# Optimization experiments

Hardware: AMD Instinct MI355X
Metric: run time of the kernel (lower is better)

The kernel has to match this reference:

```python
import jax, jax.numpy as jnp
import numpy as np

S, B, D_MODEL, H, DH = 2048, 2, 1024, 16, 64
FACTOR = 1.0 / np.sqrt(DH).astype(np.float32)


def setup_inputs() -> dict:
    key = jax.random.key(0)
    ks = jax.random.split(key, 12)
    sc = 0.02
    inp = {
        'query': jax.random.normal(ks[0], (S, B, D_MODEL), jnp.float32),
        'key': jax.random.normal(ks[1], (S, B, D_MODEL), jnp.float32),
        'value': jax.random.normal(ks[2], (S, B, D_MODEL), jnp.float32),
        # causal mask [seq_q, seq_k, 1]; 0 -> masked
        'mask': jnp.tril(jnp.ones((S, S), dtype=bool))[:, :, None],
        'Wq': jax.random.normal(ks[3], (H * DH, D_MODEL), jnp.float32) * sc,
        'bq': jnp.zeros((H * DH,), jnp.float32),
        'Wk': jax.random.normal(ks[4], (H * DH, D_MODEL), jnp.float32) * sc,
        'bk': jnp.zeros((H * DH,), jnp.float32),
        'Wv': jax.random.normal(ks[5], (H * DH, D_MODEL), jnp.float32) * sc,
        'bv': jnp.zeros((H * DH,), jnp.float32),
        'Wo': jax.random.normal(ks[6], (D_MODEL, H * DH), jnp.float32) * sc,
        'bo': jnp.zeros((D_MODEL,), jnp.float32),
    }
    return inp


def _split_heads(x):
    # pattern: 's b (head_dim head_num) -> s b head_num head_dim' (head_dim is OUTER)
    s, b, _ = x.shape
    return x.reshape(s, b, DH, H).transpose(0, 1, 3, 2)  # [s,b,H,DH]


def reference(query, key, value, mask, Wq, bq, Wk, bk, Wv, bv, Wo, bo):
    q = _split_heads(query @ Wq.T + bq)
    k = _split_heads(key @ Wk.T + bk)
    v = _split_heads(value @ Wv.T + bv)
    scores = jnp.einsum('ibhd,jbhd->ijbh', q, k) * FACTOR  # [i,j,b,h]
    scores = jnp.where(mask[..., None], scores, -jnp.inf)
    attn = jax.nn.softmax(scores, axis=1)  # softmax over keys (dim=1)
    out = jnp.einsum('ijbh,jbhd->ibhd', attn, v)  # [i,b,h,d]
    out = out.reshape(S, B, H * DH)  # 'i b h d -> i b (h d)'
    return out @ Wo.T + bo
```

## Files before the change

kernel.cpp:

```cpp
#include <hip/hip_runtime.h>


typedef float f32x4 __attribute__((ext_vector_type(4)));
typedef float f32x16 __attribute__((ext_vector_type(16)));
typedef __bf16 bf16x8_t __attribute__((ext_vector_type(8)));
typedef unsigned short ushort8 __attribute__((ext_vector_type(8)));
typedef unsigned int uint4v __attribute__((ext_vector_type(4)));
typedef unsigned int uint2v __attribute__((ext_vector_type(2)));

#define S_LEN 2048
#define BATCH 2
#define DMODEL 1024
#define NHEAD 16
#define DHEAD 64
#define K_SCALE 0.18033688011112042f

__device__ __forceinline__ unsigned short f2bf(float x) {
  unsigned int u = __builtin_bit_cast(unsigned int, x);
  u += 0x7fffu + ((u >> 16) & 1u);
  return (unsigned short)(u >> 16);
}

__device__ __forceinline__ f32x4 mfma16(ushort8 a, ushort8 b, f32x4 c) {
  return __builtin_amdgcn_mfma_f32_16x16x32_bf16(
      __builtin_bit_cast(bf16x8_t, a), __builtin_bit_cast(bf16x8_t, b), c, 0, 0, 0);
}
__device__ __forceinline__ f32x16 mfma32(ushort8 a, ushort8 b, f32x16 c) {
  return __builtin_amdgcn_mfma_f32_32x32x16_bf16(
      __builtin_bit_cast(bf16x8_t, a), __builtin_bit_cast(bf16x8_t, b), c, 0, 0, 0);
}

__device__ __forceinline__ ushort8 pack8(float4 a, float4 b, float s) {
  ushort8 t;
  t[0] = f2bf(a.x * s); t[1] = f2bf(a.y * s); t[2] = f2bf(a.z * s); t[3] = f2bf(a.w * s);
  t[4] = f2bf(b.x * s); t[5] = f2bf(b.y * s); t[6] = f2bf(b.z * s); t[7] = f2bf(b.w * s);
  return t;
}

__device__ __forceinline__ void gload16(unsigned short* lds, const unsigned short* g) {
  __builtin_amdgcn_global_load_lds(
      (const __attribute__((address_space(1))) unsigned int*)g,
      (__attribute__((address_space(3))) unsigned int*)lds, 16, 0, 0);
}

__global__ __launch_bounds__(256) void cvt_kernel(
    const float* __restrict__ q, const float* __restrict__ k, const float* __restrict__ v,
    const float* __restrict__ wq, const float* __restrict__ wk,
    const float* __restrict__ wv, const float* __restrict__ wo,
    unsigned short* __restrict__ qB, unsigned short* __restrict__ kB,
    unsigned short* __restrict__ vB, unsigned short* __restrict__ wqB,
    unsigned short* __restrict__ wkB, unsigned short* __restrict__ wvB,
    unsigned short* __restrict__ woB)
{
  const int c = blockIdx.x * 256 + threadIdx.x;
  const float* s; unsigned short* d; int base;
  if      (c < 524288)  { s = q;  d = qB;  base = 0; }
  else if (c < 1048576) { s = k;  d = kB;  base = 524288; }
  else if (c < 1572864) { s = v;  d = vB;  base = 1048576; }
  else if (c < 1703936) { s = wq; d = wqB; base = 1572864; }
  else if (c < 1835008) { s = wk; d = wkB; base = 1703936; }
  else if (c < 1966080) { s = wv; d = wvB; base = 1835008; }
  else                  { s = wo; d = woB; base = 1966080; }
  const size_t off = (size_t)(c - base) * 8;
  const float4 v0 = *reinterpret_cast<const float4*>(s + off);
  const float4 v1 = *reinterpret_cast<const float4*>(s + off + 4);
  *reinterpret_cast<ushort8*>(d + off) = pack8(v0, v1, 1.0f);
}

template<bool OUTBF16>
__global__ __launch_bounds__(256) void gemm_bf16_kernel(
    const unsigned short* __restrict__ A, const unsigned short* __restrict__ W,
    const float* __restrict__ bias, void* __restrict__ Cv, float oscale)
{
  __shared__ __align__(16) unsigned short As[2][128 * 64];
  __shared__ __align__(16) unsigned short Ws[2][64 * 64];
  const int tid = threadIdx.x;
  const int lane = tid & 63;
  const int w = tid >> 6;
  const int wm = (w >> 1) * 64, wn = (w & 1) * 32;
  const int g = lane >> 4, lr = lane & 15;

  const int bid = (int)blockIdx.x;
  const int widx = (bid & 7) * 64 + (bid >> 3);
  const int n0 = (widx & 15) * 64;
  const int m0 = (widx >> 4) * 128;

  f32x4 acc[4][2] = {};

#define STAGE(buf, k0)                                                              \
  {                                                                                 \
    _Pragma("unroll")                                                               \
    for (int ii = 0; ii < 4; ++ii) {                                                \
      const int c = ii * 256 + tid;                                                 \
      const int row = c >> 3;                                                       \
      const int sl = (c & 7) ^ (row & 7);                                           \
      gload16(&As[buf][c * 8], A + (size_t)(m0 + row) * DMODEL + (k0) + sl * 8);    \
    }                                                                               \
    _Pragma("unroll")                                                               \
    for (int ii = 0; ii < 2; ++ii) {                                                \
      const int c = ii * 256 + tid;                                                 \
      const int row = c >> 3;                                                       \
      const int sl = (c & 7) ^ (row & 7);                                           \
      gload16(&Ws[buf][c * 8], W + (size_t)(n0 + row) * DMODEL + (k0) + sl * 8);    \
    }                                                                               \
  }

  STAGE(0, 0);
  int cur = 0;

  for (int t = 0; t < 16; ++t) {
    __syncthreads();
    if (t < 15) STAGE(cur ^ 1, (t + 1) * 64);

    const char* ab = (const char*)&As[cur][0];
    const char* wb = (const char*)&Ws[cur][0];
#pragma unroll
    for (int kk = 0; kk < 2; ++kk) {
      ushort8 af[4], bw[2];
#pragma unroll
      for (int mt = 0; mt < 4; ++mt) {
        const int row = wm + mt * 16 + lr;
        af[mt] = *reinterpret_cast<const ushort8*>(
            ab + row * 128 + (((kk * 4 + g) ^ (row & 7)) << 4));
      }
#pragma unroll
      for (int nt = 0; nt < 2; ++nt) {
        const int row = wn + nt * 16 + lr;
        bw[nt] = *reinterpret_cast<const ushort8*>(
            wb + row * 128 + (((kk * 4 + g) ^ (row & 7)) << 4));
      }
      __builtin_amdgcn_s_setprio(1);
#pragma unroll
      for (int mt = 0; mt < 4; ++mt)
#pragma unroll
        for (int nt = 0; nt < 2; ++nt)
          acc[mt][nt] = mfma16(af[mt], bw[nt], acc[mt][nt]);
      __builtin_amdgcn_s_setprio(0);
    }
    cur ^= 1;
  }
#undef STAGE

#pragma unroll
  for (int nt = 0; nt < 2; ++nt) {
    const int col = n0 + wn + nt * 16 + lr;
    const float bv = bias[col];
#pragma unroll
    for (int mt = 0; mt < 4; ++mt)
#pragma unroll
      for (int r = 0; r < 4; ++r) {
        const int rowg = m0 + wm + mt * 16 + g * 4 + r;
        const float vv = (acc[mt][nt][r] + bv) * oscale;
        if constexpr (OUTBF16)
          ((unsigned short*)Cv)[(size_t)rowg * DMODEL + col] = f2bf(vv);
        else
          ((float*)Cv)[(size_t)rowg * DMODEL + col] = vv;
      }
  }
}

__global__ __launch_bounds__(256) void head_tr0_kernel(
    const unsigned short* __restrict__ in, unsigned short* __restrict__ out)
{
  __shared__ __align__(16) unsigned short T[32 * 256];
  const int tid = threadIdx.x;
  const int n0 = blockIdx.x * 32, o0 = blockIdx.y * 256;
#pragma unroll
  for (int i = 0; i < 4; ++i) {
    const int c = i * 256 + tid;
    const int row = c >> 5, c8 = c & 31;
    ushort8 v = *reinterpret_cast<const ushort8*>(in + (size_t)(n0 + row) * DMODEL + o0 + c8 * 8);
    int y = (row * 512 + c8 * 16) ^ ((row & 3) << 5);
    *reinterpret_cast<ushort8*>((char*)T + y) = v;
  }
  __syncthreads();
  const int d0 = o0 >> 4, s0 = n0 >> 1;
#pragma unroll
  for (int rep = 0; rep < 2; ++rep) {
    const int e = rep * 256 + tid;
    const int hh = e & 15, s = (e >> 4) & 15, b = (e >> 8) & 1;
    const int n = s * 2 + b;
    unsigned short vals[16];
#pragma unroll
    for (int dd = 0; dd < 16; ++dd) {
      int y = n * 512 + ((dd * 32 + hh * 2) ^ ((n & 3) << 5));
      vals[dd] = *(const unsigned short*)((const char*)T + y);
    }
    uint4v w0, w1;
#pragma unroll
    for (int j = 0; j < 4; ++j) {
      w0[j] = (unsigned)vals[2 * j] | ((unsigned)vals[2 * j + 1] << 16);
      w1[j] = (unsigned)vals[8 + 2 * j] | ((unsigned)vals[8 + 2 * j + 1] << 16);
    }
    unsigned short* dst = out + ((size_t)(b * 16 + hh) * S_LEN + s0 + s) * DHEAD + d0;
    *reinterpret_cast<uint4v*>(dst) = w0;
    *reinterpret_cast<uint4v*>(dst + 8) = w1;
  }
}

__global__ __launch_bounds__(256) void head_tr1_kernel(
    const unsigned short* __restrict__ in, unsigned short* __restrict__ out)
{
  __shared__ __align__(16) unsigned short T[64 * 64];
  const int tid = threadIdx.x;
  const int n0 = blockIdx.x * 64, o0 = blockIdx.y * 64;
#pragma unroll
  for (int i = 0; i < 2; ++i) {
    const int c = i * 256 + tid;
    const int row = c >> 3, c8 = c & 7;
    ushort8 v = *reinterpret_cast<const ushort8*>(in + (size_t)(n0 + row) * DMODEL + o0 + c8 * 8);
    int y = (row * 128 + c8 * 16) ^ ((row & 7) << 4);
    *reinterpret_cast<ushort8*>((char*)T + y) = v;
  }
  __syncthreads();
  const int d0 = o0 >> 4, s0 = n0 >> 1;
  const int shalf = tid & 1, seg = tid >> 1;
  const int dd = seg & 3, hh = (seg >> 2) & 15, b = (seg >> 6) & 1;
  unsigned short vals[16];
#pragma unroll
  for (int i = 0; i < 16; ++i) {
    const int s = shalf * 16 + i;
    const int n = s * 2 + b;
    int y = n * 128 + (((dd * 16 + hh) * 2) ^ ((n & 7) << 4));
    vals[i] = *(const unsigned short*)((const char*)T + y);
  }
  uint4v w0, w1;
#pragma unroll
  for (int j = 0; j < 4; ++j) {
    w0[j] = (unsigned)vals[2 * j] | ((unsigned)vals[2 * j + 1] << 16);
    w1[j] = (unsigned)vals[8 + 2 * j] | ((unsigned)vals[8 + 2 * j + 1] << 16);
  }
  unsigned short* dst = out + ((size_t)(b * 16 + hh) * DHEAD + d0 + dd) * S_LEN + s0 + shalf * 16;
  *reinterpret_cast<uint4v*>(dst) = w0;
  *reinterpret_cast<uint4v*>(dst + 8) = w1;
}

__global__ __launch_bounds__(256, 4) void attn_part_kernel(
    const unsigned short* __restrict__ Qh, const unsigned short* __restrict__ Kh,
    const unsigned short* __restrict__ Vh, unsigned short* __restrict__ Opart,
    float* __restrict__ mlbuf)
{
  __shared__ __align__(16) unsigned short Ks[2][64 * 64];
  __shared__ __align__(16) unsigned short Vs[2][64 * 64];

  const int tid = threadIdx.x;
  const int lane = tid & 63;
  const int w = tid >> 6;
  const int ln31 = lane & 31;
  const int hf = lane >> 5;

  const int u = 39 - (int)blockIdx.x;
  int Q, c;
  if      (u < 4)  { Q = u;                 c = 0; }
  else if (u < 12) { Q = 4 + ((u - 4) >> 1);  c = (u - 4) & 1; }
  else if (u < 24) { Q = 8 + (u - 12) / 3;    c = (u - 12) % 3; }
  else             { Q = 12 + ((u - 24) >> 2); c = (u - 24) & 3; }
  int off;
  if      (Q < 4)  off = Q;
  else if (Q < 8)  off = 4 + (Q - 4) * 2;
  else if (Q < 12) off = 12 + (Q - 8) * 3;
  else             off = 24 + (Q - 12) * 4;

  const int hb = blockIdx.y;
  const int head = hb & 15, b = hb >> 4;
  const int slot = hb * 40 + off + c;
  const int t0 = c * 8;
  const int tmax = 2 * Q + 1;
  const int t1 = (tmax < t0 + 7) ? tmax : (t0 + 7);
  const int q0 = Q * 128;

  const size_t hoff = (size_t)(b * NHEAD + head) * (S_LEN * DHEAD);
  const unsigned short* Qg = Qh + hoff;
  const unsigned short* Kg = Kh + hoff;
  const unsigned short* Vg = Vh + hoff;

  const int qwb = q0 + w * 32;
  const int qg = qwb + ln31;

  ushort8 qf[4];
#pragma unroll
  for (int kt = 0; kt < 4; ++kt)
    qf[kt] = *reinterpret_cast<const ushort8*>(Qg + (size_t)qg * DHEAD + kt * 16 + hf * 8);

  f32x16 oa0 = {0}, oa1 = {0};
  float mrun = -1e30f, ssum = 0.f;

#define STAGE(buf, kv)                                                             \
  {                                                                                \
    _Pragma("unroll")                                                              \
    for (int ii = 0; ii < 2; ++ii) {                                               \
      const int c2 = ii * 256 + tid;                                               \
      const int row = c2 >> 3;                                                     \
      const int sl = (c2 & 7) ^ (row & 7);                                         \
      gload16(&Ks[buf][c2 * 8], Kg + (size_t)((kv) + row) * 64 + sl * 8);          \
    }                                                                              \
    _Pragma("unroll")                                                              \
    for (int ii = 0; ii < 2; ++ii) {                                               \
      const int c2 = ii * 256 + tid;                                               \
      const int row = c2 >> 3;                                                     \
      const int sl = (c2 & 7) ^ (row & 7);                                         \
      gload16(&Vs[buf][c2 * 8], Vg + (size_t)row * S_LEN + (kv) + sl * 8);         \
    }                                                                              \
  }

  STAGE(0, t0 * 64);
  int cur = 0;

  const int kb0 = ln31 * 128 + ((hf * 16) ^ ((ln31 & 7) << 4));
  const int kb1 = (32 + ln31) * 128 + ((hf * 16) ^ ((ln31 & 7) << 4));

  for (int t = t0; t <= t1; ++t) {
    const int kv0 = t * 64;
    __syncthreads();
    if (t < t1) STAGE(cur ^ 1, kv0 + 64);

    if (kv0 <= qwb + 31) {
      f32x16 sc0 = {0}, sc1 = {0};
      {
        const char* ksb = (const char*)&Ks[cur][0];
        __builtin_amdgcn_s_setprio(1);
#pragma unroll
        for (int kt = 0; kt < 4; ++kt) {
          ushort8 kf0 = *reinterpret_cast<const ushort8*>(ksb + (kb0 ^ (kt << 5)));
          ushort8 kf1 = *reinterpret_cast<const ushort8*>(ksb + (kb1 ^ (kt << 5)));
          sc0 = mfma32(kf0, qf[kt], sc0);
          sc1 = mfma32(kf1, qf[kt], sc1);
        }
        __builtin_amdgcn_s_setprio(0);
      }

      if (kv0 + 63 > qwb) {
#pragma unroll
        for (int r = 0; r < 16; ++r) {
          const int keyb = kv0 + (r & 3) + 8 * (r >> 2) + 4 * hf;
          if (keyb > qg) sc0[r] = -1e30f;
          if (keyb + 32 > qg) sc1[r] = -1e30f;
        }
      }

      float pmax = sc0[0];
#pragma unroll
      for (int r = 1; r < 16; ++r) pmax = fmaxf(pmax, sc0[r]);
#pragma unroll
      for (int r = 0; r < 16; ++r) pmax = fmaxf(pmax, sc1[r]);
      pmax = fmaxf(pmax, __shfl_xor(pmax, 32, 64));

      if (!__all(pmax <= mrun + 8.0f)) {
        const float mnew = fmaxf(mrun, pmax);
        const float scl = exp2f(mrun - mnew);
        ssum *= scl;
#pragma unroll
        for (int r = 0; r < 16; ++r) { oa0[r] *= scl; oa1[r] *= scl; }
        mrun = mnew;
      }

      float pv0[16], pv1[16];
      float psum = 0.f;
#pragma unroll
      for (int r = 0; r < 16; ++r) {
        pv0[r] = exp2f(sc0[r] - mrun);
        pv1[r] = exp2f(sc1[r] - mrun);
        psum += pv0[r] + pv1[r];
      }
      psum += __shfl_xor(psum, 32, 64);
      ssum += psum;

      unsigned int cc[16], pc[16];
#pragma unroll
      for (int j = 0; j < 8; ++j) {
        asm("v_cvt_pk_bf16_f32 %0, %1, %2" : "=v"(cc[j]) : "v"(pv0[2 * j]), "v"(pv0[2 * j + 1]));
        asm("v_cvt_pk_bf16_f32 %0, %1, %2" : "=v"(cc[8 + j]) : "v"(pv1[2 * j]), "v"(pv1[2 * j + 1]));
      }
#pragma unroll
      for (int j = 0; j < 16; ++j)
        pc[j] = (unsigned int)__shfl_xor((int)cc[j], 32, 64);

      uint4v pfw[4];
#pragma unroll
      for (int mt = 0; mt < 2; ++mt) {
#pragma unroll
        for (int ktl = 0; ktl < 2; ++ktl) {
          const int o = mt * 8 + ktl * 4;
          uint4v u4;
          u4[0] = hf ? pc[o + 2] : cc[o + 0];
          u4[1] = hf ? pc[o + 3] : cc[o + 1];
          u4[2] = hf ? cc[o + 2] : pc[o + 0];
          u4[3] = hf ? cc[o + 3] : pc[o + 1];
          pfw[mt * 2 + ktl] = u4;
        }
      }

      {
        const char* vsb = (const char*)&Vs[cur][0];
        __builtin_amdgcn_s_setprio(1);
#pragma unroll
        for (int kt = 0; kt < 4; ++kt) {
          ushort8 vf0 = *reinterpret_cast<const ushort8*>(vsb + (kb0 ^ (kt << 5)));
          ushort8 vf1 = *reinterpret_cast<const ushort8*>(vsb + (kb1 ^ (kt << 5)));
          ushort8 pfr = __builtin_bit_cast(ushort8, pfw[kt]);
          oa0 = mfma32(vf0, pfr, oa0);
          oa1 = mfma32(vf1, pfr, oa1);
        }
        __builtin_amdgcn_s_setprio(0);
      }
    }

    cur ^= 1;
  }
#undef STAGE

  const int ql = w * 32 + ln31;
  unsigned short* ob = Opart + (size_t)slot * 8192 + ql * 64;
#pragma unroll
  for (int mt2 = 0; mt2 < 2; ++mt2) {
#pragma unroll
    for (int rq = 0; rq < 4; ++rq) {
      const int dd = mt2 * 32 + 8 * rq + 4 * hf;
      const f32x16& a = mt2 ? oa1 : oa0;
      unsigned int w0, w1;
      asm("v_cvt_pk_bf16_f32 %0, %1, %2" : "=v"(w0)
          : "v"(a[4 * rq + 0]), "v"(a[4 * rq + 1]));
      asm("v_cvt_pk_bf16_f32 %0, %1, %2" : "=v"(w1)
          : "v"(a[4 * rq + 2]), "v"(a[4 * rq + 3]));
      uint2v pk = { w0, w1 };
      *reinterpret_cast<uint2v*>(ob + dd) = pk;
    }
  }
  if (hf == 0) {
    mlbuf[slot * 256 + ql] = mrun;
    mlbuf[slot * 256 + 128 + ql] = ssum;
  }
}

__global__ __launch_bounds__(256) void attn_combine_kernel(
    const unsigned short* __restrict__ Opart, const float* __restrict__ mlbuf,
    unsigned short* __restrict__ O)
{
  const int Q = blockIdx.x, hb = blockIdx.y;
  const int head = hb & 15, b = hb >> 4;
  const int nch = (2 * Q + 1) / 8 + 1;
  int off;
  if      (Q < 4)  off = Q;
  else if (Q < 8)  off = 4 + (Q - 4) * 2;
  else if (Q < 12) off = 12 + (Q - 8) * 3;
  else             off = 24 + (Q - 12) * 4;
  const int s0 = hb * 40 + off;

  const int tid = threadIdx.x;
  const int q = tid >> 1, dh = (tid & 1) * 32;

  float mc[4], lc[4];
  float M = -1e30f;
  for (int cc = 0; cc < nch; ++cc) {
    mc[cc] = mlbuf[(s0 + cc) * 256 + q];
    lc[cc] = mlbuf[(s0 + cc) * 256 + 128 + q];
    M = fmaxf(M, mc[cc]);
  }
  float L = 0.f, wgt[4];
  for (int cc = 0; cc < nch; ++cc) {
    wgt[cc] = exp2f(mc[cc] - M);
    L += wgt[cc] * lc[cc];
  }
  const float invL = 1.0f / L;

  float acc[32] = {};
  for (int cc = 0; cc < nch; ++cc) {
    const unsigned short* p = Opart + (size_t)(s0 + cc) * 8192 + q * 64 + dh;
    const float wv = wgt[cc];
#pragma unroll
    for (int seg = 0; seg < 4; ++seg) {
      ushort8 v = *reinterpret_cast<const ushort8*>(p + seg * 8);
#pragma unroll
      for (int j = 0; j < 8; ++j) {
        const float f = __builtin_bit_cast(float, ((unsigned int)v[j]) << 16);
        acc[seg * 8 + j] += wv * f;
      }
    }
  }

  unsigned int wpk[16];
#pragma unroll
  for (int j = 0; j < 16; ++j) {
    asm("v_cvt_pk_bf16_f32 %0, %1, %2" : "=v"(wpk[j])
        : "v"(acc[2 * j] * invL), "v"(acc[2 * j + 1] * invL));
  }
  unsigned short* dst = O + ((size_t)((Q * 128 + q) * BATCH + b)) * DMODEL + head * DHEAD + dh;
#pragma unroll
  for (int seg = 0; seg < 4; ++seg)
    *reinterpret_cast<uint4v*>(dst + seg * 8) =
        uint4v{ wpk[4 * seg], wpk[4 * seg + 1], wpk[4 * seg + 2], wpk[4 * seg + 3] };
}

extern "C" void kernel_launch(void* const* d_in, const int* in_sizes, int n_in,
                              void* d_out, int out_size, void* d_ws, size_t ws_size,
                              hipStream_t stream)
{
  (void)in_sizes; (void)n_in; (void)out_size; (void)ws_size;
  const float* query = (const float*)d_in[0];
  const float* key_  = (const float*)d_in[1];
  const float* value = (const float*)d_in[2];
  const float* Wq = (const float*)d_in[4];
  const float* bq = (const float*)d_in[5];
  const float* Wk = (const float*)d_in[6];
  const float* bk = (const float*)d_in[7];
  const float* Wv = (const float*)d_in[8];
  const float* bv = (const float*)d_in[9];
  const float* Wo = (const float*)d_in[10];
  const float* bo = (const float*)d_in[11];
  float* out = (float*)d_out;

  const size_t NE = (size_t)4096 * DMODEL;
  const size_t NW = (size_t)DMODEL * DMODEL;
  unsigned short* qB  = (unsigned short*)d_ws;
  unsigned short* kB  = qB + NE;
  unsigned short* vB  = kB + NE;
  unsigned short* g1  = vB + NE;
  unsigned short* Qh  = g1 + NE;
  unsigned short* Kh  = Qh + NE;
  unsigned short* Vh  = Kh + NE;
  unsigned short* wqB = Vh + NE;
  unsigned short* wkB = wqB + NW;
  unsigned short* wvB = wkB + NW;
  unsigned short* woB = wvB + NW;
  unsigned short* aO  = qB;
  unsigned short* Opart = kB;
  float* mlbuf = (float*)(kB + (size_t)1280 * 8192);

  dim3 t0grid(128, 4);
  dim3 t1grid(64, 16);

  cvt_kernel<<<dim3(8192), 256, 0, stream>>>(query, key_, value, Wq, Wk, Wv, Wo,
                                             qB, kB, vB, wqB, wkB, wvB, woB);
  gemm_bf16_kernel<true><<<dim3(512), 256, 0, stream>>>(qB, wqB, bq, g1, 1.0f);
  head_tr0_kernel<<<t0grid, 256, 0, stream>>>(g1, Qh);
  gemm_bf16_kernel<true><<<dim3(512), 256, 0, stream>>>(kB, wkB, bk, g1, K_SCALE);
  head_tr0_kernel<<<t0grid, 256, 0, stream>>>(g1, Kh);
  gemm_bf16_kernel<true><<<dim3(512), 256, 0, stream>>>(vB, wvB, bv, g1, 1.0f);
  head_tr1_kernel<<<t1grid, 256, 0, stream>>>(g1, Vh);
  attn_part_kernel<<<dim3(40, 32), 256, 0, stream>>>(Qh, Kh, Vh, Opart, mlbuf);
  attn_combine_kernel<<<dim3(16, 32), 256, 0, stream>>>(Opart, mlbuf, aO);
  gemm_bf16_kernel<false><<<dim3(512), 256, 0, stream>>>(aO, woB, bo, out, 1.0f);
}
```

Measured before the change: 156.4 us.

## Replace LDS double-buffer with register-staged prefetch and single LDS buffer

Replaces the async global-to-LDS double buffer with a register prefetch of the next K/V tile, written into a single LDS buffer after compute, with two barriers per iteration. Halving LDS use lets launch bounds rise to 5 blocks per SM for more occupancy. It also rewrites the row-max and row-sum reductions as trees of max3 and pairwise adds to shorten dependency chains. The cost is extra VGPRs for the staged tiles, an extra barrier per iteration, and less overlap between loads and compute.

```diff
diff --git a/kernel.cpp b/kernel.cpp
--- a/kernel.cpp
+++ b/kernel.cpp
@@ -28,6 +28,10 @@
 __device__ __forceinline__ f32x16 mfma32(ushort8 a, ushort8 b, f32x16 c) {
   return __builtin_amdgcn_mfma_f32_32x32x16_bf16(
       __builtin_bit_cast(bf16x8_t, a), __builtin_bit_cast(bf16x8_t, b), c, 0, 0, 0);
+}
+
+__device__ __forceinline__ float max3f(float a, float b, float c) {
+  return fmaxf(fmaxf(a, b), c);
 }
 
 __device__ __forceinline__ ushort8 pack8(float4 a, float4 b, float s) {
@@ -235,13 +239,13 @@
   *reinterpret_cast<uint4v*>(dst + 8) = w1;
 }
 
-__global__ __launch_bounds__(256, 4) void attn_part_kernel(
+__global__ __launch_bounds__(256, 5) void attn_part_kernel(
     const unsigned short* __restrict__ Qh, const unsigned short* __restrict__ Kh,
     const unsigned short* __restrict__ Vh, unsigned short* __restrict__ Opart,
     float* __restrict__ mlbuf)
 {
-  __shared__ __align__(16) unsigned short Ks[2][64 * 64];
-  __shared__ __align__(16) unsigned short Vs[2][64 * 64];
+  __shared__ __align__(16) unsigned short Ks[64 * 64];
+  __shared__ __align__(16) unsigned short Vs[64 * 64];
 
   const int tid = threadIdx.x;
   const int lane = tid & 63;
@@ -285,39 +289,42 @@
   f32x16 oa0 = {0}, oa1 = {0};
   float mrun = -1e30f, ssum = 0.f;
 
-#define STAGE(buf, kv)                                                             \
-  {                                                                                \
-    _Pragma("unroll")                                                              \
-    for (int ii = 0; ii < 2; ++ii) {                                               \
-      const int c2 = ii * 256 + tid;                                               \
-      const int row = c2 >> 3;                                                     \
-      const int sl = (c2 & 7) ^ (row & 7);                                         \
-      gload16(&Ks[buf][c2 * 8], Kg + (size_t)((kv) + row) * 64 + sl * 8);          \
-    }                                                                              \
-    _Pragma("unroll")                                                              \
-    for (int ii = 0; ii < 2; ++ii) {                                               \
-      const int c2 = ii * 256 + tid;                                               \
-      const int row = c2 >> 3;                                                     \
-      const int sl = (c2 & 7) ^ (row & 7);                                         \
-      gload16(&Vs[buf][c2 * 8], Vg + (size_t)row * S_LEN + (kv) + sl * 8);         \
-    }                                                                              \
-  }
-
-  STAGE(0, t0 * 64);
-  int cur = 0;
+  ushort8 sK0, sK1, sV0, sV1;
+  const int r0 = tid >> 3, f0 = tid & 7;
+  const int r1 = r0 + 32;
+  const int dK0 = r0 * 128 + ((f0 ^ (r0 & 7)) << 4);
+  const int dK1 = r1 * 128 + ((f0 ^ (r1 & 7)) << 4);
+
+#define LOAD_REGS(kv)                                                               \
+  {                                                                                 \
+    sK0 = *reinterpret_cast<const ushort8*>(Kg + (size_t)((kv) + r0) * 64 + f0 * 8);\
+    sK1 = *reinterpret_cast<const ushort8*>(Kg + (size_t)((kv) + r1) * 64 + f0 * 8);\
+    sV0 = *reinterpret_cast<const ushort8*>(Vg + (size_t)r0 * S_LEN + (kv) + f0 * 8);\
+    sV1 = *reinterpret_cast<const ushort8*>(Vg + (size_t)r1 * S_LEN + (kv) + f0 * 8);\
+  }
+#define WRITE_LDS()                                                                 \
+  {                                                                                 \
+    *reinterpret_cast<ushort8*>((char*)Ks + dK0) = sK0;                             \
+    *reinterpret_cast<ushort8*>((char*)Ks + dK1) = sK1;                             \
+    *reinterpret_cast<ushort8*>((char*)Vs + dK0) = sV0;                             \
+    *reinterpret_cast<ushort8*>((char*)Vs + dK1) = sV1;                             \
+  }
+
+  LOAD_REGS(t0 * 64);
+  WRITE_LDS();
+  __syncthreads();
 
   const int kb0 = ln31 * 128 + ((hf * 16) ^ ((ln31 & 7) << 4));
   const int kb1 = (32 + ln31) * 128 + ((hf * 16) ^ ((ln31 & 7) << 4));
 
   for (int t = t0; t <= t1; ++t) {
     const int kv0 = t * 64;
-    __syncthreads();
-    if (t < t1) STAGE(cur ^ 1, kv0 + 64);
+    if (t < t1) LOAD_REGS(kv0 + 64);
 
     if (kv0 <= qwb + 31) {
       f32x16 sc0 = {0}, sc1 = {0};
       {
-        const char* ksb = (const char*)&Ks[cur][0];
+        const char* ksb = (const char*)Ks;
         __builtin_amdgcn_s_setprio(1);
 #pragma unroll
         for (int kt = 0; kt < 4; ++kt) {
@@ -338,11 +345,22 @@
         }
       }
 
-      float pmax = sc0[0];
-#pragma unroll
-      for (int r = 1; r < 16; ++r) pmax = fmaxf(pmax, sc0[r]);
-#pragma unroll
-      for (int r = 0; r < 16; ++r) pmax = fmaxf(pmax, sc1[r]);
+      float m0a = max3f(sc0[0], sc0[1], sc0[2]);
+      float m1a = max3f(sc0[3], sc0[4], sc0[5]);
+      float m2a = max3f(sc0[6], sc0[7], sc0[8]);
+      float m3a = max3f(sc0[9], sc0[10], sc0[11]);
+      float m4a = max3f(sc0[12], sc0[13], sc0[14]);
+      float m5a = max3f(sc0[15], sc1[0], sc1[1]);
+      float m6a = max3f(sc1[2], sc1[3], sc1[4]);
+      float m7a = max3f(sc1[5], sc1[6], sc1[7]);
+      float m8a = max3f(sc1[8], sc1[9], sc1[10]);
+      float m9a = max3f(sc1[11], sc1[12], sc1[13]);
+      float mAa = fmaxf(sc1[14], sc1[15]);
+      float n0a = max3f(m0a, m1a, m2a);
+      float n1a = max3f(m3a, m4a, m5a);
+      float n2a = max3f(m6a, m7a, m8a);
+      float n3a = fmaxf(m9a, mAa);
+      float pmax = fmaxf(max3f(n0a, n1a, n2a), n3a);
       pmax = fmaxf(pmax, __shfl_xor(pmax, 32, 64));
 
       if (!__all(pmax <= mrun + 8.0f)) {
@@ -355,13 +373,18 @@
       }
 
       float pv0[16], pv1[16];
-      float psum = 0.f;
 #pragma unroll
       for (int r = 0; r < 16; ++r) {
         pv0[r] = exp2f(sc0[r] - mrun);
         pv1[r] = exp2f(sc1[r] - mrun);
-        psum += pv0[r] + pv1[r];
-      }
+      }
+      float a8[8];
+#pragma unroll
+      for (int r = 0; r < 8; ++r)
+        a8[r] = (pv0[r] + pv0[r + 8]) + (pv1[r] + pv1[r + 8]);
+      float a4_0 = a8[0] + a8[4], a4_1 = a8[1] + a8[5];
+      float a4_2 = a8[2] + a8[6], a4_3 = a8[3] + a8[7];
+      float psum = (a4_0 + a4_1) + (a4_2 + a4_3);
       psum += __shfl_xor(psum, 32, 64);
       ssum += psum;
 
@@ -391,7 +414,7 @@
       }
 
       {
-        const char* vsb = (const char*)&Vs[cur][0];
+        const char* vsb = (const char*)Vs;
         __builtin_amdgcn_s_setprio(1);
 #pragma unroll
         for (int kt = 0; kt < 4; ++kt) {
@@ -405,9 +428,12 @@
       }
     }
 
-    cur ^= 1;
-  }
-#undef STAGE
+    __syncthreads();
+    if (t < t1) WRITE_LDS();
+    __syncthreads();
+  }
+#undef LOAD_REGS
+#undef WRITE_LDS
 
   const int ql = w * 32 + ln31;
   unsigned short* ob = Opart + (size_t)slot * 8192 + ql * 64;
```

After: 199.4 us (median of 2 runs). 27.5% more time.

## Fuse QKV GEMMs, permute Wq/Wk rows to drop head transposes, skip masked tiles

Applied to the files above, without the earlier changes.

The Q and K weight rows are permuted during conversion so the projection GEMM writes Q and K already grouped by head. This removes the two head_tr0 transpose kernels, and attention reads Q and K with strided row indexing instead. The three projection GEMMs merge into one launch over blockIdx.z. Inside attention, the upper 32-key half of each tile is skipped on diagonal tiles where it is fully masked, which cuts MFMA, exp and shuffle work; the max reduction is also tree-structured. The strided Q/K loads may reduce memory coalescing in the attention kernel.

```diff
diff --git a/kernel.cpp b/kernel.cpp
--- a/kernel.cpp
+++ b/kernel.cpp
@@ -28,6 +28,21 @@
 __device__ __forceinline__ f32x16 mfma32(ushort8 a, ushort8 b, f32x16 c) {
   return __builtin_amdgcn_mfma_f32_32x32x16_bf16(
       __builtin_bit_cast(bf16x8_t, a), __builtin_bit_cast(bf16x8_t, b), c, 0, 0, 0);
+}
+
+__device__ __forceinline__ float max3f(float a, float b, float c) {
+  return fmaxf(fmaxf(a, b), c);
+}
+
+__device__ __forceinline__ float tmax16(const f32x16& s) {
+  float a = max3f(s[0], s[1], s[2]);
+  float b_ = max3f(s[3], s[4], s[5]);
+  float c_ = max3f(s[6], s[7], s[8]);
+  float d_ = max3f(s[9], s[10], s[11]);
+  float e_ = max3f(s[12], s[13], s[14]);
+  float f_ = max3f(a, b_, s[15]);
+  float g_ = fmaxf(c_, d_);
+  return max3f(f_, g_, e_);
 }
 
 __device__ __forceinline__ ushort8 pack8(float4 a, float4 b, float s) {
@@ -53,27 +68,48 @@
     unsigned short* __restrict__ woB)
 {
   const int c = blockIdx.x * 256 + threadIdx.x;
-  const float* s; unsigned short* d; int base;
+  const float* s; unsigned short* d; int base; bool perm = false;
   if      (c < 524288)  { s = q;  d = qB;  base = 0; }
   else if (c < 1048576) { s = k;  d = kB;  base = 524288; }
   else if (c < 1572864) { s = v;  d = vB;  base = 1048576; }
-  else if (c < 1703936) { s = wq; d = wqB; base = 1572864; }
-  else if (c < 1835008) { s = wk; d = wkB; base = 1703936; }
+  else if (c < 1703936) { s = wq; d = wqB; base = 1572864; perm = true; }
+  else if (c < 1835008) { s = wk; d = wkB; base = 1703936; perm = true; }
   else if (c < 1966080) { s = wv; d = wvB; base = 1835008; }
   else                  { s = wo; d = woB; base = 1966080; }
-  const size_t off = (size_t)(c - base) * 8;
-  const float4 v0 = *reinterpret_cast<const float4*>(s + off);
-  const float4 v1 = *reinterpret_cast<const float4*>(s + off + 4);
-  *reinterpret_cast<ushort8*>(d + off) = pack8(v0, v1, 1.0f);
-}
-
-template<bool OUTBF16>
-__global__ __launch_bounds__(256) void gemm_bf16_kernel(
-    const unsigned short* __restrict__ A, const unsigned short* __restrict__ W,
-    const float* __restrict__ bias, void* __restrict__ Cv, float oscale)
+  const size_t cc_ = (size_t)(c - base);
+  const size_t src = cc_ * 8;
+  size_t dst = src;
+  if (perm) {
+    const int o = (int)(cc_ >> 7);
+    const int colc = (int)(cc_ & 127);
+    const int op = ((o & 15) << 6) | (o >> 4);
+    dst = ((size_t)op << 10) + (size_t)colc * 8;
+  }
+  const float4 v0 = *reinterpret_cast<const float4*>(s + src);
+  const float4 v1 = *reinterpret_cast<const float4*>(s + src + 4);
+  *reinterpret_cast<ushort8*>(d + dst) = pack8(v0, v1, 1.0f);
+}
+
+__global__ __launch_bounds__(256) void gemm_qkv_kernel(
+    const unsigned short* __restrict__ qA, const unsigned short* __restrict__ kA,
+    const unsigned short* __restrict__ vA,
+    const unsigned short* __restrict__ wqW, const unsigned short* __restrict__ wkW,
+    const unsigned short* __restrict__ wvW,
+    const float* __restrict__ bq, const float* __restrict__ bk,
+    const float* __restrict__ bv,
+    unsigned short* __restrict__ Cq, unsigned short* __restrict__ Ck,
+    unsigned short* __restrict__ Cv)
 {
   __shared__ __align__(16) unsigned short As[2][128 * 64];
   __shared__ __align__(16) unsigned short Ws[2][64 * 64];
+  const int z = blockIdx.z;
+  const unsigned short* A = (z == 0) ? qA : (z == 1) ? kA : vA;
+  const unsigned short* W = (z == 0) ? wqW : (z == 1) ? wkW : wvW;
+  const float* bias = (z == 0) ? bq : (z == 1) ? bk : bv;
+  unsigned short* C = (z == 0) ? Cq : (z == 1) ? Ck : Cv;
+  const float oscale = (z == 1) ? K_SCALE : 1.0f;
+  const bool pbias = (z < 2);
+
   const int tid = threadIdx.x;
   const int lane = tid & 63;
   const int w = tid >> 6;
@@ -144,57 +180,102 @@
 #pragma unroll
   for (int nt = 0; nt < 2; ++nt) {
     const int col = n0 + wn + nt * 16 + lr;
-    const float bv = bias[col];
+    const int bidx = pbias ? (((col & 63) << 4) | (col >> 6)) : col;
+    const float bvv = bias[bidx];
 #pragma unroll
     for (int mt = 0; mt < 4; ++mt)
 #pragma unroll
       for (int r = 0; r < 4; ++r) {
         const int rowg = m0 + wm + mt * 16 + g * 4 + r;
-        const float vv = (acc[mt][nt][r] + bv) * oscale;
-        if constexpr (OUTBF16)
-          ((unsigned short*)Cv)[(size_t)rowg * DMODEL + col] = f2bf(vv);
-        else
-          ((float*)Cv)[(size_t)rowg * DMODEL + col] = vv;
-      }
-  }
-}
-
-__global__ __launch_bounds__(256) void head_tr0_kernel(
-    const unsigned short* __restrict__ in, unsigned short* __restrict__ out)
+        C[(size_t)rowg * DMODEL + col] = f2bf((acc[mt][nt][r] + bvv) * oscale);
+      }
+  }
+}
+
+__global__ __launch_bounds__(256) void gemm_out_kernel(
+    const unsigned short* __restrict__ A, const unsigned short* __restrict__ W,
+    const float* __restrict__ bias, float* __restrict__ C)
 {
-  __shared__ __align__(16) unsigned short T[32 * 256];
+  __shared__ __align__(16) unsigned short As[2][128 * 64];
+  __shared__ __align__(16) unsigned short Ws[2][64 * 64];
   const int tid = threadIdx.x;
-  const int n0 = blockIdx.x * 32, o0 = blockIdx.y * 256;
-#pragma unroll
-  for (int i = 0; i < 4; ++i) {
-    const int c = i * 256 + tid;
-    const int row = c >> 5, c8 = c & 31;
-    ushort8 v = *reinterpret_cast<const ushort8*>(in + (size_t)(n0 + row) * DMODEL + o0 + c8 * 8);
-    int y = (row * 512 + c8 * 16) ^ ((row & 3) << 5);
-    *reinterpret_cast<ushort8*>((char*)T + y) = v;
-  }
-  __syncthreads();
-  const int d0 = o0 >> 4, s0 = n0 >> 1;
-#pragma unroll
-  for (int rep = 0; rep < 2; ++rep) {
-    const int e = rep * 256 + tid;
-    const int hh = e & 15, s = (e >> 4) & 15, b = (e >> 8) & 1;
-    const int n = s * 2 + b;
-    unsigned short vals[16];
-#pragma unroll
-    for (int dd = 0; dd < 16; ++dd) {
-      int y = n * 512 + ((dd * 32 + hh * 2) ^ ((n & 3) << 5));
-      vals[dd] = *(const unsigned short*)((const char*)T + y);
+  const int lane = tid & 63;
+  const int w = tid >> 6;
+  const int wm = (w >> 1) * 64, wn = (w & 1) * 32;
+  const int g = lane >> 4, lr = lane & 15;
+
+  const int bid = (int)blockIdx.x;
+  const int widx = (bid & 7) * 64 + (bid >> 3);
+  const int n0 = (widx & 15) * 64;
+  const int m0 = (widx >> 4) * 128;
+
+  f32x4 acc[4][2] = {};
+
+#define STAGE(buf, k0)                                                              \
+  {                                                                                 \
+    _Pragma("unroll")                                                               \
+    for (int ii = 0; ii < 4; ++ii) {                                                \
+      const int c = ii * 256 + tid;                                                 \
+      const int row = c >> 3;                                                       \
+      const int sl = (c & 7) ^ (row & 7);                                           \
+      gload16(&As[buf][c * 8], A + (size_t)(m0 + row) * DMODEL + (k0) + sl * 8);    \
+    }                                                                               \
+    _Pragma("unroll")                                                               \
+    for (int ii = 0; ii < 2; ++ii) {                                                \
+      const int c = ii * 256 + tid;                                                 \
+      const int row = c >> 3;                                                       \
+      const int sl = (c & 7) ^ (row & 7);                                           \
+      gload16(&Ws[buf][c * 8], W + (size_t)(n0 + row) * DMODEL + (k0) + sl * 8);    \
+    }                                                                               \
+  }
+
+  STAGE(0, 0);
+  int cur = 0;
+
+  for (int t = 0; t < 16; ++t) {
+    __syncthreads();
+    if (t < 15) STAGE(cur ^ 1, (t + 1) * 64);
+
+    const char* ab = (const char*)&As[cur][0];
+    const char* wb = (const char*)&Ws[cur][0];
+#pragma unroll
+    for (int kk = 0; kk < 2; ++kk) {
+      ushort8 af[4], bw[2];
+#pragma unroll
+      for (int mt = 0; mt < 4; ++mt) {
+        const int row = wm + mt * 16 + lr;
+        af[mt] = *reinterpret_cast<const ushort8*>(
+            ab + row * 128 + (((kk * 4 + g) ^ (row & 7)) << 4));
+      }
+#pragma unroll
+      for (int nt = 0; nt < 2; ++nt) {
+        const int row = wn + nt * 16 + lr;
+        bw[nt] = *reinterpret_cast<const ushort8*>(
+            wb + row * 128 + (((kk * 4 + g) ^ (row & 7)) << 4));
+      }
+      __builtin_amdgcn_s_setprio(1);
+#pragma unroll
+      for (int mt = 0; mt < 4; ++mt)
+#pragma unroll
+        for (int nt = 0; nt < 2; ++nt)
+          acc[mt][nt] = mfma16(af[mt], bw[nt], acc[mt][nt]);
+      __builtin_amdgcn_s_setprio(0);
     }
-    uint4v w0, w1;
-#pragma unroll
-    for (int j = 0; j < 4; ++j) {
-      w0[j] = (unsigned)vals[2 * j] | ((unsigned)vals[2 * j + 1] << 16);
-      w1[j] = (unsigned)vals[8 + 2 * j] | ((unsigned)vals[8 + 2 * j + 1] << 16);
-    }
-    unsigned short* dst = out + ((size_t)(b * 16 + hh) * S_LEN + s0 + s) * DHEAD + d0;
-    *reinterpret_cast<uint4v*>(dst) = w0;
-    *reinterpret_cast<uint4v*>(dst + 8) = w1;
+    cur ^= 1;
+  }
+#undef STAGE
+
+#pragma unroll
+  for (int nt = 0; nt < 2; ++nt) {
+    const int col = n0 + wn + nt * 16 + lr;
+    const float bvv = bias[col];
+#pragma unroll
+    for (int mt = 0; mt < 4; ++mt)
+#pragma unroll
+      for (int r = 0; r < 4; ++r) {
+        const int rowg = m0 + wm + mt * 16 + g * 4 + r;
+        C[(size_t)rowg * DMODEL + col] = acc[mt][nt][r] + bvv;
+      }
   }
 }
 
@@ -236,7 +317,7 @@
 }
 
 __global__ __launch_bounds__(256, 4) void attn_part_kernel(
-    const unsigned short* __restrict__ Qh, const unsigned short* __restrict__ Kh,
+    const unsigned short* __restrict__ Qn, const unsigned short* __restrict__ Kn,
     const unsigned short* __restrict__ Vh, unsigned short* __restrict__ Opart,
     float* __restrict__ mlbuf)
 {
@@ -269,10 +350,9 @@
   const int t1 = (tmax < t0 + 7) ? tmax : (t0 + 7);
   const int q0 = Q * 128;
 
-  const size_t hoff = (size_t)(b * NHEAD + head) * (S_LEN * DHEAD);
-  const unsigned short* Qg = Qh + hoff;
-  const unsigned short* Kg = Kh + hoff;
-  const unsigned short* Vg = Vh + hoff;
+  const unsigned short* Qg = Qn + head * 64;
+  const unsigned short* Kg = Kn + head * 64;
+  const unsigned short* Vg = Vh + (size_t)(b * NHEAD + head) * (S_LEN * DHEAD);
 
   const int qwb = q0 + w * 32;
   const int qg = qwb + ln31;
@@ -280,7 +360,8 @@
   ushort8 qf[4];
 #pragma unroll
   for (int kt = 0; kt < 4; ++kt)
-    qf[kt] = *reinterpret_cast<const ushort8*>(Qg + (size_t)qg * DHEAD + kt * 16 + hf * 8);
+    qf[kt] = *reinterpret_cast<const ushort8*>(
+        Qg + ((size_t)(qg * 2 + b) << 10) + kt * 16 + hf * 8);
 
   f32x16 oa0 = {0}, oa1 = {0};
   float mrun = -1e30f, ssum = 0.f;
@@ -292,7 +373,8 @@
       const int c2 = ii * 256 + tid;                                               \
       const int row = c2 >> 3;                                                     \
       const int sl = (c2 & 7) ^ (row & 7);                                         \
-      gload16(&Ks[buf][c2 * 8], Kg + (size_t)((kv) + row) * 64 + sl * 8);          \
+      gload16(&Ks[buf][c2 * 8],                                                    \
+              Kg + ((size_t)((((kv) + row) << 1) + b) << 10) + sl * 8);            \
     }                                                                              \
     _Pragma("unroll")                                                              \
     for (int ii = 0; ii < 2; ++ii) {                                               \
@@ -315,6 +397,8 @@
     if (t < t1) STAGE(cur ^ 1, kv0 + 64);
 
     if (kv0 <= qwb + 31) {
+      const bool have_hi = (kv0 < qwb);
+
       f32x16 sc0 = {0}, sc1 = {0};
       {
         const char* ksb = (const char*)&Ks[cur][0];
@@ -322,27 +406,35 @@
 #pragma unroll
         for (int kt = 0; kt < 4; ++kt) {
           ushort8 kf0 = *reinterpret_cast<const ushort8*>(ksb + (kb0 ^ (kt << 5)));
-          ushort8 kf1 = *reinterpret_cast<const ushort8*>(ksb + (kb1 ^ (kt << 5)));
           sc0 = mfma32(kf0, qf[kt], sc0);
-          sc1 = mfma32(kf1, qf[kt], sc1);
+        }
+        if (have_hi) {
+#pragma unroll
+          for (int kt = 0; kt < 4; ++kt) {
+            ushort8 kf1 = *reinterpret_cast<const ushort8*>(ksb + (kb1 ^ (kt << 5)));
+            sc1 = mfma32(kf1, qf[kt], sc1);
+          }
         }
         __builtin_amdgcn_s_setprio(0);
       }
 
-      if (kv0 + 63 > qwb) {
+      if (kv0 + 31 > qwb) {
 #pragma unroll
         for (int r = 0; r < 16; ++r) {
           const int keyb = kv0 + (r & 3) + 8 * (r >> 2) + 4 * hf;
           if (keyb > qg) sc0[r] = -1e30f;
-          if (keyb + 32 > qg) sc1[r] = -1e30f;
         }
       }
-
-      float pmax = sc0[0];
-#pragma unroll
-      for (int r = 1; r < 16; ++r) pmax = fmaxf(pmax, sc0[r]);
-#pragma unroll
-      for (int r = 0; r < 16; ++r) pmax = fmaxf(pmax, sc1[r]);
+      if (have_hi && kv0 + 63 > qwb) {
+#pragma unroll
+        for (int r = 0; r < 16; ++r) {
+          const int keyb = kv0 + 32 + (r & 3) + 8 * (r >> 2) + 4 * hf;
+          if (keyb > qg) sc1[r] = -1e30f;
+        }
+      }
+
+      float pmax = tmax16(sc0);
+      if (have_hi) pmax = fmaxf(pmax, tmax16(sc1));
       pmax = fmaxf(pmax, __shfl_xor(pmax, 32, 64));
 
       if (!__all(pmax <= mrun + 8.0f)) {
@@ -355,38 +447,59 @@
       }
 
       float pv0[16], pv1[16];
-      float psum = 0.f;
-#pragma unroll
-      for (int r = 0; r < 16; ++r) {
-        pv0[r] = exp2f(sc0[r] - mrun);
-        pv1[r] = exp2f(sc1[r] - mrun);
-        psum += pv0[r] + pv1[r];
-      }
+#pragma unroll
+      for (int r = 0; r < 16; ++r) pv0[r] = exp2f(sc0[r] - mrun);
+      float s8[8];
+#pragma unroll
+      for (int r = 0; r < 8; ++r) s8[r] = pv0[r] + pv0[r + 8];
+      if (have_hi) {
+#pragma unroll
+        for (int r = 0; r < 16; ++r) pv1[r] = exp2f(sc1[r] - mrun);
+#pragma unroll
+        for (int r = 0; r < 8; ++r) s8[r] += pv1[r] + pv1[r + 8];
+      }
+      float psum = ((s8[0] + s8[4]) + (s8[1] + s8[5])) +
+                   ((s8[2] + s8[6]) + (s8[3] + s8[7]));
       psum += __shfl_xor(psum, 32, 64);
       ssum += psum;
 
       unsigned int cc[16], pc[16];
 #pragma unroll
-      for (int j = 0; j < 8; ++j) {
+      for (int j = 0; j < 8; ++j)
         asm("v_cvt_pk_bf16_f32 %0, %1, %2" : "=v"(cc[j]) : "v"(pv0[2 * j]), "v"(pv0[2 * j + 1]));
-        asm("v_cvt_pk_bf16_f32 %0, %1, %2" : "=v"(cc[8 + j]) : "v"(pv1[2 * j]), "v"(pv1[2 * j + 1]));
-      }
-#pragma unroll
-      for (int j = 0; j < 16; ++j)
+#pragma unroll
+      for (int j = 0; j < 8; ++j)
         pc[j] = (unsigned int)__shfl_xor((int)cc[j], 32, 64);
+      if (have_hi) {
+#pragma unroll
+        for (int j = 0; j < 8; ++j)
+          asm("v_cvt_pk_bf16_f32 %0, %1, %2" : "=v"(cc[8 + j]) : "v"(pv1[2 * j]), "v"(pv1[2 * j + 1]));
+#pragma unroll
+        for (int j = 8; j < 16; ++j)
+          pc[j] = (unsigned int)__shfl_xor((int)cc[j], 32, 64);
+      }
 
       uint4v pfw[4];
 #pragma unroll
-      for (int mt = 0; mt < 2; ++mt) {
+      for (int ktl = 0; ktl < 2; ++ktl) {
+        const int o = ktl * 4;
+        uint4v u4;
+        u4[0] = hf ? pc[o + 2] : cc[o + 0];
+        u4[1] = hf ? pc[o + 3] : cc[o + 1];
+        u4[2] = hf ? cc[o + 2] : pc[o + 0];
+        u4[3] = hf ? cc[o + 3] : pc[o + 1];
+        pfw[ktl] = u4;
+      }
+      if (have_hi) {
 #pragma unroll
         for (int ktl = 0; ktl < 2; ++ktl) {
-          const int o = mt * 8 + ktl * 4;
+          const int o = 8 + ktl * 4;
           uint4v u4;
           u4[0] = hf ? pc[o + 2] : cc[o + 0];
           u4[1] = hf ? pc[o + 3] : cc[o + 1];
           u4[2] = hf ? cc[o + 2] : pc[o + 0];
           u4[3] = hf ? cc[o + 3] : pc[o + 1];
-          pfw[mt * 2 + ktl] = u4;
+          pfw[2 + ktl] = u4;
         }
       }
 
@@ -394,12 +507,22 @@
         const char* vsb = (const char*)&Vs[cur][0];
         __builtin_amdgcn_s_setprio(1);
 #pragma unroll
-        for (int kt = 0; kt < 4; ++kt) {
+        for (int kt = 0; kt < 2; ++kt) {
           ushort8 vf0 = *reinterpret_cast<const ushort8*>(vsb + (kb0 ^ (kt << 5)));
           ushort8 vf1 = *reinterpret_cast<const ushort8*>(vsb + (kb1 ^ (kt << 5)));
           ushort8 pfr = __builtin_bit_cast(ushort8, pfw[kt]);
           oa0 = mfma32(vf0, pfr, oa0);
           oa1 = mfma32(vf1, pfr, oa1);
+        }
+        if (have_hi) {
+#pragma unroll
+          for (int kt = 2; kt < 4; ++kt) {
+            ushort8 vf0 = *reinterpret_cast<const ushort8*>(vsb + (kb0 ^ (kt << 5)));
+            ushort8 vf1 = *reinterpret_cast<const ushort8*>(vsb + (kb1 ^ (kt << 5)));
+            ushort8 pfr = __builtin_bit_cast(ushort8, pfw[kt]);
+            oa0 = mfma32(vf0, pfr, oa0);
+            oa1 = mfma32(vf1, pfr, oa1);
+          }
         }
         __builtin_amdgcn_s_setprio(0);
       }
@@ -515,9 +638,9 @@
   unsigned short* kB  = qB + NE;
   unsigned short* vB  = kB + NE;
   unsigned short* g1  = vB + NE;
-  unsigned short* Qh  = g1 + NE;
-  unsigned short* Kh  = Qh + NE;
-  unsigned short* Vh  = Kh + NE;
+  unsigned short* Qn  = g1 + NE;
+  unsigned short* Kn  = Qn + NE;
+  unsigned short* Vh  = Kn + NE;
   unsigned short* wqB = Vh + NE;
   unsigned short* wkB = wqB + NW;
   unsigned short* wvB = wkB + NW;
@@ -526,18 +649,12 @@
   unsigned short* Opart = kB;
   float* mlbuf = (float*)(kB + (size_t)1280 * 8192);
 
-  dim3 t0grid(128, 4);
-  dim3 t1grid(64, 16);
-
   cvt_kernel<<<dim3(8192), 256, 0, stream>>>(query, key_, value, Wq, Wk, Wv, Wo,
                                              qB, kB, vB, wqB, wkB, wvB, woB);
-  gemm_bf16_kernel<true><<<dim3(512), 256, 0, stream>>>(qB, wqB, bq, g1, 1.0f);
-  head_tr0_kernel<<<t0grid, 256, 0, stream>>>(g1, Qh);
-  gemm_bf16_kernel<true><<<dim3(512), 256, 0, stream>>>(kB, wkB, bk, g1, K_SCALE);
-  head_tr0_kernel<<<t0grid, 256, 0, stream>>>(g1, Kh);
-  gemm_bf16_kernel<true><<<dim3(512), 256, 0, stream>>>(vB, wvB, bv, g1, 1.0f);
-  head_tr1_kernel<<<t1grid, 256, 0, stream>>>(g1, Vh);
-  attn_part_kernel<<<dim3(40, 32), 256, 0, stream>>>(Qh, Kh, Vh, Opart, mlbuf);
+  gemm_qkv_kernel<<<dim3(512, 1, 3), 256, 0, stream>>>(
+      qB, kB, vB, wqB, wkB, wvB, bq, bk, bv, Qn, Kn, g1);
+  head_tr1_kernel<<<dim3(64, 16), 256, 0, stream>>>(g1, Vh);
+  attn_part_kernel<<<dim3(40, 32), 256, 0, stream>>>(Qn, Kn, Vh, Opart, mlbuf);
   attn_combine_kernel<<<dim3(16, 32), 256, 0, stream>>>(Opart, mlbuf, aO);
-  gemm_bf16_kernel<false><<<dim3(512), 256, 0, stream>>>(aO, woB, bo, out, 1.0f);
-}
+  gemm_out_kernel<<<dim3(512), 256, 0, stream>>>(aO, woB, bo, out);
+}
```

Result: slower. 187.2 us (+19.7%).
